# Kernel tuning notes

Measured on AMD Instinct MI355X. Metric: run time of the kernel, lower is better.

The kernel has to match this reference:

```python
import jax, jax.numpy as jnp
import numpy as np

EMBED_DIM = 1024
HEAD = 16
DK = EMBED_DIM // HEAD  # 64
B, S = 2, 2048
NEG = -1.0e9


def setup_inputs() -> dict:
    key = jax.random.key(0)
    ks = jax.random.split(key, 8)
    d = {
        'query': jax.random.normal(ks[0], (B, S, EMBED_DIM), jnp.float32),
        'key': jax.random.normal(ks[1], (B, S, EMBED_DIM), jnp.float32),
        'value': jax.random.normal(ks[2], (B, S, EMBED_DIM), jnp.float32),
        'masked': jax.random.randint(ks[3], (B, S, S), 0, 2).astype(bool),
        'Wq': jax.random.normal(ks[4], (EMBED_DIM, EMBED_DIM), jnp.float32) / np.sqrt(EMBED_DIM),
        'Wk': jax.random.normal(ks[5], (EMBED_DIM, EMBED_DIM), jnp.float32) / np.sqrt(EMBED_DIM),
        'Wv': jax.random.normal(ks[6], (EMBED_DIM, EMBED_DIM), jnp.float32) / np.sqrt(EMBED_DIM),
        'Wo': jax.random.normal(ks[7], (EMBED_DIM, EMBED_DIM), jnp.float32) / np.sqrt(EMBED_DIM),
    }
    return d


def reference(query, key, value, masked, Wq, Wk, Wv, Wo):
    # projections (bias-free Linear: x @ W), split into heads: [B, H, S, DK]
    def split_heads(x):
        b, s, _ = x.shape
        return x.reshape(b, s, HEAD, DK).transpose(0, 2, 1, 3)

    q = split_heads(query @ Wq)
    k = split_heads(key @ Wk)
    v = split_heads(value @ Wv)

    scale = 1.0 / jnp.sqrt(jnp.asarray(DK, q.dtype))
    scores = jnp.einsum('bhqd,bhkd->bhqk', q, k) * scale
    scores = jnp.where(masked[:, None, :, :], NEG, scores)
    attn = jax.nn.softmax(scores, axis=-1)
    out = jnp.einsum('bhqk,bhkd->bhqd', attn, v)  # [B, H, S, DK]
    out = out.transpose(0, 2, 1, 3).reshape(query.shape[0], -1, EMBED_DIM)
    return out @ Wo
```

## Files before the change

### kernel.cpp

```cpp
#include <hip/hip_runtime.h>
#include <hip/hip_bf16.h>

typedef float f32x4 __attribute__((ext_vector_type(4)));
typedef __bf16 bf16x8 __attribute__((ext_vector_type(8)));

__device__ __forceinline__ unsigned short f2bf(float f){
  unsigned int u = __builtin_bit_cast(unsigned int, f);
  u += 0x7fffu + ((u >> 16) & 1u);
  return (unsigned short)(u >> 16);
}
__device__ __forceinline__ float bf2f(unsigned short h){
  return __builtin_bit_cast(float, (unsigned int)h << 16);
}

__device__ __forceinline__ void glds16(const void* g, void* l){
  __builtin_amdgcn_global_load_lds((const __attribute__((address_space(1))) void*)g,
                                   (__attribute__((address_space(3))) void*)l, 16, 0, 0);
}

__device__ __forceinline__ f32x4 mfma16(bf16x8 a, bf16x8 b, f32x4 c){
  return __builtin_amdgcn_mfma_f32_16x16x32_bf16(a, b, c, 0, 0, 0);
}

#if __has_builtin(__builtin_amdgcn_exp2f)
__device__ __forceinline__ float exp2v(float x){ return __builtin_amdgcn_exp2f(x); }
#else
__device__ __forceinline__ float exp2v(float x){ return exp2f(x); }
#endif

__device__ __forceinline__ unsigned int cvtpk(float a, float b){
  unsigned int r;
  asm("v_cvt_pk_bf16_f32 %0, %1, %2" : "=v"(r) : "v"(a), "v"(b));
  return r;
}

__global__ void detect_kernel(const unsigned int* __restrict__ m, int* __restrict__ flag){
  int t = threadIdx.x;
  int bad = 0;
  for(int i = t; i < 4096; i += 256) bad |= (m[i] > 1u);
  unsigned long long b = __ballot(bad != 0);
  __shared__ int sbuf[4];
  if((t & 63) == 0) sbuf[t >> 6] = (b != 0ull);
  __syncthreads();
  if(t == 0) flag[0] = (sbuf[0] | sbuf[1] | sbuf[2] | sbuf[3]) ? 0 : 1;
}

__global__ void pack_mask_kernel(const unsigned char* __restrict__ m8,
                                 unsigned int* __restrict__ mp,
                                 const int* __restrict__ flag){
  const int wid = threadIdx.x >> 6, lane = threadIdx.x & 63;
  const int row = blockIdx.x * 4 + wid;
  const int is32 = flag[0];
  const int* m32 = (const int*)m8;
  for(int c0 = 0; c0 < 2048; c0 += 64){
    int mv = is32 ? m32[(size_t)row*2048 + c0 + lane]
                  : (int)m8[(size_t)row*2048 + c0 + lane];
    unsigned long long b = __ballot(mv != 0);
    if(lane == 0){
      mp[(size_t)row*64 + (c0 >> 5)]     = (unsigned int)b;
      mp[(size_t)row*64 + (c0 >> 5) + 1] = (unsigned int)(b >> 32);
    }
  }
}

__global__ void cvt3_kernel(const float* __restrict__ qs, const float* __restrict__ ks,
                            const float* __restrict__ vs, unsigned short* __restrict__ dst){
  const float* src = (blockIdx.y==0)?qs:(blockIdx.y==1)?ks:vs;
  unsigned short* d = dst + (size_t)blockIdx.y * 4194304;
  int i = blockIdx.x * 256 + threadIdx.x;
  const float4* s = (const float4*)src;
  float4 a = s[2*i], b = s[2*i+1];
  union { unsigned short h[8]; uint4 v; } o;
  o.h[0]=f2bf(a.x); o.h[1]=f2bf(a.y); o.h[2]=f2bf(a.z); o.h[3]=f2bf(a.w);
  o.h[4]=f2bf(b.x); o.h[5]=f2bf(b.y); o.h[6]=f2bf(b.z); o.h[7]=f2bf(b.w);
  ((uint4*)d)[i] = o.v;
}

__global__ void transW_kernel(const float* __restrict__ Wq, const float* __restrict__ Wk,
                              const float* __restrict__ Wv, const float* __restrict__ Wo,
                              unsigned short* __restrict__ WT){
  const float* W = (blockIdx.y==0)?Wq:(blockIdx.y==1)?Wk:(blockIdx.y==2)?Wv:Wo;
  const float scale = (blockIdx.y==0) ? 0.1803368801111601f : 1.0f;
  unsigned short* D = WT + (size_t)blockIdx.y * 1048576;
  int r0 = (blockIdx.x >> 4) * 64, c0 = (blockIdx.x & 15) * 64;
  __shared__ unsigned short T[64][65];
  int t = threadIdx.x;
  {
    int r = t >> 2, cb = (t & 3) * 16;
    const float4* src = (const float4*)(W + (size_t)(r0 + r) * 1024 + (c0 + cb));
    float4 v0 = src[0], v1 = src[1], v2 = src[2], v3 = src[3];
    float vals[16] = {v0.x,v0.y,v0.z,v0.w, v1.x,v1.y,v1.z,v1.w,
                      v2.x,v2.y,v2.z,v2.w, v3.x,v3.y,v3.z,v3.w};
    #pragma unroll
    for(int j=0;j<16;j++) T[cb + j][r] = f2bf(vals[j] * scale);
  }
  __syncthreads();
  {
    int c = t >> 2, rb = (t & 3) * 16;
    union { unsigned short h[16]; uint4 v[2]; } o;
    #pragma unroll
    for(int j=0;j<16;j++) o.h[j] = T[c][rb + j];
    uint4* dp = (uint4*)(D + (size_t)(c0 + c) * 1024 + (r0 + rb));
    dp[0] = o.v[0]; dp[1] = o.v[1];
  }
}

template<int OUTF32>
__global__ __launch_bounds__(256,2) void gemm_bt(
    const unsigned short* __restrict__ A0, const unsigned short* __restrict__ A1, const unsigned short* __restrict__ A2,
    const unsigned short* __restrict__ B0, const unsigned short* __restrict__ B1, const unsigned short* __restrict__ B2,
    unsigned short* __restrict__ C0, unsigned short* __restrict__ C1, unsigned short* __restrict__ C2,
    float* __restrict__ Cf)
{
  const unsigned short* A  = (blockIdx.z==0)?A0:(blockIdx.z==1)?A1:A2;
  const unsigned short* BT = (blockIdx.z==0)?B0:(blockIdx.z==1)?B1:B2;
  unsigned short* C        = (blockIdx.z==0)?C0:(blockIdx.z==1)?C1:C2;
  __shared__ unsigned short Asm[128*64];
  __shared__ unsigned short Bsm[128*64];
  const int wid = threadIdx.x >> 6, lane = threadIdx.x & 63;
  const int m0 = blockIdx.x * 128, n0 = blockIdx.y * 128;
  const int wrow = wid >> 1, wcol = wid & 1;
  const int li = lane & 15, lg = lane >> 4, li7 = lane & 7;
  f32x4 acc[4][4] = {};
  const int sr = lane >> 3;
  const int sc = lane & 7;

  for(int kt = 0; kt < 16; ++kt){
    const int kofs = kt * 64;
    #pragma unroll
    for(int i=0;i<4;i++){
      int r = wid*32 + i*8 + sr;
      int blk = sc ^ sr;
      glds16(A  + (size_t)(m0 + r)*1024 + kofs + blk*8, &Asm[(wid*32 + i*8)*64]);
      glds16(BT + (size_t)(n0 + r)*1024 + kofs + blk*8, &Bsm[(wid*32 + i*8)*64]);
    }
    __syncthreads();
    #pragma unroll
    for(int kk=0; kk<2; kk++){
      bf16x8 af[4], bfv[4];
      #pragma unroll
      for(int fm=0; fm<4; fm++){
        int row = wrow*64 + fm*16 + li;
        int blk = (kk*4 + lg) ^ li7;
        af[fm] = *(const bf16x8*)&Asm[row*64 + blk*8];
      }
      #pragma unroll
      for(int fn=0; fn<4; fn++){
        int row = wcol*64 + fn*16 + li;
        int blk = (kk*4 + lg) ^ li7;
        bfv[fn] = *(const bf16x8*)&Bsm[row*64 + blk*8];
      }
      __builtin_amdgcn_s_setprio(1);
      #pragma unroll
      for(int fm=0; fm<4; fm++)
        #pragma unroll
        for(int fn=0; fn<4; fn++)
          acc[fm][fn] = mfma16(af[fm], bfv[fn], acc[fm][fn]);
      __builtin_amdgcn_s_setprio(0);
    }
    __syncthreads();
  }
  if(OUTF32 == 0 && blockIdx.z == 2){
    #pragma unroll
    for(int fm=0; fm<4; fm++){
      #pragma unroll
      for(int fn=0; fn<4; fn++){
        int col  = n0 + wcol*64 + fn*16 + li;
        int rowb = m0 + wrow*64 + fm*16 + lg*4;
        int bq = rowb >> 11, s = rowb & 2047;
        union { unsigned short h[4]; unsigned long long u; } o;
        #pragma unroll
        for(int r=0;r<4;r++) o.h[r] = f2bf(acc[fm][fn][r]);
        *(unsigned long long*)&C[((size_t)(bq*16 + (col>>6))*64 + (col&63))*2048 + s] = o.u;
      }
    }
  } else {
    #pragma unroll
    for(int fm=0; fm<4; fm++){
      #pragma unroll
      for(int fn=0; fn<4; fn++){
        int col  = n0 + wcol*64 + fn*16 + li;
        int rowb = m0 + wrow*64 + fm*16 + lg*4;
        #pragma unroll
        for(int r=0;r<4;r++){
          if(OUTF32) Cf[(size_t)(rowb + r)*1024 + col] = acc[fm][fn][r];
          else       C [(size_t)(rowb + r)*1024 + col] = f2bf(acc[fm][fn][r]);
        }
      }
    }
  }
}

__global__ __launch_bounds__(256,4) void attn_kernel(
    const unsigned short* __restrict__ Q, const unsigned short* __restrict__ K,
    const unsigned short* __restrict__ Vt, unsigned short* __restrict__ O,
    const unsigned int* __restrict__ mp)
{
  __shared__ unsigned short Ksm[2][64*64];
  __shared__ unsigned short Vsm[2][64*64];
  const int wid = threadIdx.x >> 6, lane = threadIdx.x & 63;
  const int orig = blockIdx.x;
  const int wg = (orig & 7) * 128 + (orig >> 3);
  const int qt = wg & 31, bh = wg >> 5;
  const int b = bh >> 4, h = bh & 15;
  const int q0 = qt * 64;
  const int li = lane & 15, lg = lane >> 4;
  const int li7 = li & 7;
  const int src0 = li + 32*(lg & 1);
  const int src1 = src0 + 16;
  const int hiSel = lg >> 1;

  bf16x8 qf[2];
  {
    const unsigned short* qp = Q + (size_t)(b*2048 + q0 + wid*16 + li)*1024 + h*64 + lg*8;
    qf[0] = *(const bf16x8*)qp;
    qf[1] = *(const bf16x8*)(qp + 32);
  }

  f32x4 oacc[4] = {};
  float lrow = 0.f;

  const int srow = lane >> 3;
  const int sblk = (lane & 7) ^ srow;
  const int mrowg = b*2048 + q0 + wid*16 + li;

  #pragma unroll
  for(int i=0;i<2;i++){
    int r = wid*16 + i*8 + srow;
    glds16(K  + (size_t)(b*2048 + r)*1024 + h*64 + sblk*8, &Ksm[0][(wid*16 + i*8)*64]);
    glds16(Vt + (size_t)(bh*64 + r)*2048 + sblk*8,         &Vsm[0][(wid*16 + i*8)*64]);
  }
  uint2 mw = *(const uint2*)&mp[(size_t)mrowg*64];
  uint2 mwn;
  __syncthreads();

  int buf = 0;
  for(int t = 0; t < 32; ++t){
    const int kv0 = t * 64;
    if(t < 31){
      #pragma unroll
      for(int i=0;i<2;i++){
        int r = wid*16 + i*8 + srow;
        glds16(K  + (size_t)(b*2048 + kv0 + 64 + r)*1024 + h*64 + sblk*8, &Ksm[buf^1][(wid*16 + i*8)*64]);
        glds16(Vt + (size_t)(bh*64 + r)*2048 + kv0 + 64 + sblk*8,         &Vsm[buf^1][(wid*16 + i*8)*64]);
      }
      mwn = *(const uint2*)&mp[(size_t)mrowg*64 + (size_t)((kv0 + 64) >> 5)];
    }
    float p[4][4];
    __builtin_amdgcn_s_setprio(1);
    #pragma unroll
    for(int f=0; f<4; f++){
      f32x4 s = {0.f,0.f,0.f,0.f};
      #pragma unroll
      for(int kf=0; kf<2; kf++){
        int blk = (kf*4 + lg) ^ li7;
        bf16x8 kfr = *(const bf16x8*)&Ksm[buf][(f*16 + li)*64 + blk*8];
        s = mfma16(kfr, qf[kf], s);
      }
      #pragma unroll
      for(int j=0;j<4;j++) p[f][j] = s[j];
    }
    __builtin_amdgcn_s_setprio(0);
    unsigned int Af[4], Bf[4];
    {
      float rs = 0.f;
      #pragma unroll
      for(int f=0; f<4; f++){
        unsigned int w = (f < 2) ? mw.x : mw.y;
        float e[4];
        #pragma unroll
        for(int j=0;j<4;j++){
          unsigned int bit = (w >> ((f & 1)*16 + lg*4 + j)) & 1u;
          float v = exp2v(p[f][j]);
          e[j] = bit ? 0.f : v;
          rs += e[j];
        }
        Af[f] = cvtpk(e[0], e[1]);
        Bf[f] = cvtpk(e[2], e[3]);
      }
      lrow += rs;
    }
    #pragma unroll
    for(int ks=0; ks<2; ks++){
      unsigned int a0 = __shfl(Af[ks*2],   src0);
      unsigned int a1 = __shfl(Af[ks*2+1], src0);
      unsigned int b0 = __shfl(Bf[ks*2],   src0);
      unsigned int b1 = __shfl(Bf[ks*2+1], src0);
      unsigned int c0 = __shfl(Af[ks*2],   src1);
      unsigned int c1 = __shfl(Af[ks*2+1], src1);
      unsigned int d0 = __shfl(Bf[ks*2],   src1);
      unsigned int d1 = __shfl(Bf[ks*2+1], src1);
      union { unsigned int w[4]; bf16x8 v; } pa;
      pa.w[0] = hiSel ? a1 : a0;
      pa.w[1] = hiSel ? b1 : b0;
      pa.w[2] = hiSel ? c1 : c0;
      pa.w[3] = hiSel ? d1 : d0;
      __builtin_amdgcn_s_setprio(1);
      #pragma unroll
      for(int d=0; d<4; d++){
        int blk = (ks*4 + lg) ^ li7;
        bf16x8 vf = *(const bf16x8*)&Vsm[buf][(d*16 + li)*64 + blk*8];
        oacc[d] = mfma16(pa.v, vf, oacc[d]);
      }
      __builtin_amdgcn_s_setprio(0);
    }
    __syncthreads();
    mw = mwn;
    buf ^= 1;
  }
  float rs = lrow;
  rs += __shfl_xor(rs, 16);
  rs += __shfl_xor(rs, 32);
  float inv = 1.0f / rs;
  float io0 = __shfl(inv, lg*4 + 0);
  float io1 = __shfl(inv, lg*4 + 1);
  float io2 = __shfl(inv, lg*4 + 2);
  float io3 = __shfl(inv, lg*4 + 3);
  #pragma unroll
  for(int d=0; d<4; d++){
    size_t rb = (size_t)(b*2048 + q0 + wid*16 + lg*4);
    O[(rb+0)*1024 + h*64 + 16*d + li] = f2bf(oacc[d][0] * io0);
    O[(rb+1)*1024 + h*64 + 16*d + li] = f2bf(oacc[d][1] * io1);
    O[(rb+2)*1024 + h*64 + 16*d + li] = f2bf(oacc[d][2] * io2);
    O[(rb+3)*1024 + h*64 + 16*d + li] = f2bf(oacc[d][3] * io3);
  }
}

extern "C" void kernel_launch(void* const* d_in, const int* in_sizes, int n_in,
                              void* d_out, int out_size, void* d_ws, size_t ws_size,
                              hipStream_t stream)
{
  const float* q_in = (const float*)d_in[0];
  const float* k_in = (const float*)d_in[1];
  const float* v_in = (const float*)d_in[2];
  const unsigned char* mask = (const unsigned char*)d_in[3];
  const float* Wq = (const float*)d_in[4];
  const float* Wk = (const float*)d_in[5];
  const float* Wv = (const float*)d_in[6];
  const float* Wo = (const float*)d_in[7];

  char* ws = (char*)d_ws;
  const size_t MB = 1024*1024;
  int* flag          = (int*)ws;
  unsigned short* XQ = (unsigned short*)(ws + 256);
  unsigned short* XK = (unsigned short*)(ws + 256 + 8*MB);
  unsigned short* XV = (unsigned short*)(ws + 256 + 16*MB);
  unsigned short* WT = (unsigned short*)(ws + 256 + 24*MB);
  unsigned short* Qb = (unsigned short*)(ws + 256 + 32*MB);
  unsigned short* Kb = (unsigned short*)(ws + 256 + 40*MB);
  unsigned short* Vt = (unsigned short*)(ws + 256 + 48*MB);
  unsigned short* Ob = XQ;
  unsigned int*   mpk= (unsigned int*)XV;

  detect_kernel<<<1, 256, 0, stream>>>((const unsigned int*)mask, flag);
  cvt3_kernel<<<dim3(2048,3), 256, 0, stream>>>(q_in, k_in, v_in, XQ);
  transW_kernel<<<dim3(256,4), 256, 0, stream>>>(Wq, Wk, Wv, Wo, WT);
  gemm_bt<0><<<dim3(32,8,3), 256, 0, stream>>>(XQ, XK, XV,
                                               WT, WT + 1048576, WT + 2097152,
                                               Qb, Kb, Vt, nullptr);
  pack_mask_kernel<<<1024, 256, 0, stream>>>(mask, mpk, flag);
  attn_kernel<<<1024, 256, 0, stream>>>(Qb, Kb, Vt, Ob, mpk);
  gemm_bt<1><<<dim3(32,8,1), 256, 0, stream>>>(Ob, Ob, Ob,
                                               WT + 3*1048576, WT + 3*1048576, WT + 3*1048576,
                                               nullptr, nullptr, nullptr, (float*)d_out);
}
```

Measured before the change: 153.0 us.

## Process two query row tiles per wave and use fp16 PV MFMA without shuffles

Each attention workgroup now covers 128 query rows, with each wave handling two 16-row tiles, so every K/V tile staged in LDS is reused twice and the grid halves. Softmax probabilities are packed as fp16 and fed to the 16x16x16 f16 MFMA in the layout they already have. This removes the cross-lane shuffle permutation that the bf16 path needed. V is now written as fp16 by the projection GEMM to match. The cost is more registers (launch bounds lowered to 2), fewer blocks in flight, and fp16 range/precision for V and P.

```diff
diff --git a/kernel.cpp b/kernel.cpp
--- a/kernel.cpp
+++ b/kernel.cpp
@@ -3,6 +3,8 @@
 
 typedef float f32x4 __attribute__((ext_vector_type(4)));
 typedef __bf16 bf16x8 __attribute__((ext_vector_type(8)));
+typedef _Float16 f16x2 __attribute__((ext_vector_type(2)));
+typedef _Float16 f16x4 __attribute__((ext_vector_type(4)));
 
 __device__ __forceinline__ unsigned short f2bf(float f){
   unsigned int u = __builtin_bit_cast(unsigned int, f);
@@ -13,6 +15,10 @@
   return __builtin_bit_cast(float, (unsigned int)h << 16);
 }
 
+__device__ __forceinline__ f16x2 pkrtz(float a, float b){
+  return __builtin_bit_cast(f16x2, __builtin_amdgcn_cvt_pkrtz(a, b));
+}
+
 __device__ __forceinline__ void glds16(const void* g, void* l){
   __builtin_amdgcn_global_load_lds((const __attribute__((address_space(1))) void*)g,
                                    (__attribute__((address_space(3))) void*)l, 16, 0, 0);
@@ -20,6 +26,9 @@
 
 __device__ __forceinline__ f32x4 mfma16(bf16x8 a, bf16x8 b, f32x4 c){
   return __builtin_amdgcn_mfma_f32_16x16x32_bf16(a, b, c, 0, 0, 0);
+}
+__device__ __forceinline__ f32x4 mfma16h(f16x4 a, f16x4 b, f32x4 c){
+  return __builtin_amdgcn_mfma_f32_16x16x16f16(a, b, c, 0, 0, 0);
 }
 
 #if __has_builtin(__builtin_amdgcn_exp2f)
@@ -27,12 +36,6 @@
 #else
 __device__ __forceinline__ float exp2v(float x){ return exp2f(x); }
 #endif
-
-__device__ __forceinline__ unsigned int cvtpk(float a, float b){
-  unsigned int r;
-  asm("v_cvt_pk_bf16_f32 %0, %1, %2" : "=v"(r) : "v"(a), "v"(b));
-  return r;
-}
 
 __global__ void detect_kernel(const unsigned int* __restrict__ m, int* __restrict__ flag){
   int t = threadIdx.x;
@@ -168,9 +171,9 @@
         int col  = n0 + wcol*64 + fn*16 + li;
         int rowb = m0 + wrow*64 + fm*16 + lg*4;
         int bq = rowb >> 11, s = rowb & 2047;
-        union { unsigned short h[4]; unsigned long long u; } o;
-        #pragma unroll
-        for(int r=0;r<4;r++) o.h[r] = f2bf(acc[fm][fn][r]);
+        union { f16x2 h2[2]; unsigned long long u; } o;
+        o.h2[0] = pkrtz(acc[fm][fn][0], acc[fm][fn][1]);
+        o.h2[1] = pkrtz(acc[fm][fn][2], acc[fm][fn][3]);
         *(unsigned long long*)&C[((size_t)(bq*16 + (col>>6))*64 + (col&63))*2048 + s] = o.u;
       }
     }
@@ -191,7 +194,7 @@
   }
 }
 
-__global__ __launch_bounds__(256,4) void attn_kernel(
+__global__ __launch_bounds__(256,2) void attn_kernel(
     const unsigned short* __restrict__ Q, const unsigned short* __restrict__ K,
     const unsigned short* __restrict__ Vt, unsigned short* __restrict__ O,
     const unsigned int* __restrict__ mp)
@@ -200,29 +203,29 @@
   __shared__ unsigned short Vsm[2][64*64];
   const int wid = threadIdx.x >> 6, lane = threadIdx.x & 63;
   const int orig = blockIdx.x;
-  const int wg = (orig & 7) * 128 + (orig >> 3);
-  const int qt = wg & 31, bh = wg >> 5;
+  const int wg = (orig & 7) * 64 + (orig >> 3);
+  const int qt = wg & 15, bh = wg >> 4;
   const int b = bh >> 4, h = bh & 15;
-  const int q0 = qt * 64;
+  const int q0 = qt * 128;
   const int li = lane & 15, lg = lane >> 4;
   const int li7 = li & 7;
-  const int src0 = li + 32*(lg & 1);
-  const int src1 = src0 + 16;
-  const int hiSel = lg >> 1;
-
-  bf16x8 qf[2];
+
+  const int rowA = b*2048 + q0 + wid*32 + li;
+  const int rowB = rowA + 16;
+
+  bf16x8 qfA[2], qfB[2];
   {
-    const unsigned short* qp = Q + (size_t)(b*2048 + q0 + wid*16 + li)*1024 + h*64 + lg*8;
-    qf[0] = *(const bf16x8*)qp;
-    qf[1] = *(const bf16x8*)(qp + 32);
-  }
-
-  f32x4 oacc[4] = {};
-  float lrow = 0.f;
+    const unsigned short* qa = Q + (size_t)rowA*1024 + h*64 + lg*8;
+    const unsigned short* qb = Q + (size_t)rowB*1024 + h*64 + lg*8;
+    qfA[0] = *(const bf16x8*)qa; qfA[1] = *(const bf16x8*)(qa + 32);
+    qfB[0] = *(const bf16x8*)qb; qfB[1] = *(const bf16x8*)(qb + 32);
+  }
+
+  f32x4 oaccA[4] = {}, oaccB[4] = {};
+  float lrowA = 0.f, lrowB = 0.f;
 
   const int srow = lane >> 3;
   const int sblk = (lane & 7) ^ srow;
-  const int mrowg = b*2048 + q0 + wid*16 + li;
 
   #pragma unroll
   for(int i=0;i<2;i++){
@@ -230,8 +233,9 @@
     glds16(K  + (size_t)(b*2048 + r)*1024 + h*64 + sblk*8, &Ksm[0][(wid*16 + i*8)*64]);
     glds16(Vt + (size_t)(bh*64 + r)*2048 + sblk*8,         &Vsm[0][(wid*16 + i*8)*64]);
   }
-  uint2 mw = *(const uint2*)&mp[(size_t)mrowg*64];
-  uint2 mwn;
+  uint2 mwA = *(const uint2*)&mp[(size_t)rowA*64];
+  uint2 mwB = *(const uint2*)&mp[(size_t)rowB*64];
+  uint2 mwAn, mwBn;
   __syncthreads();
 
   int buf = 0;
@@ -244,85 +248,76 @@
         glds16(K  + (size_t)(b*2048 + kv0 + 64 + r)*1024 + h*64 + sblk*8, &Ksm[buf^1][(wid*16 + i*8)*64]);
         glds16(Vt + (size_t)(bh*64 + r)*2048 + kv0 + 64 + sblk*8,         &Vsm[buf^1][(wid*16 + i*8)*64]);
       }
-      mwn = *(const uint2*)&mp[(size_t)mrowg*64 + (size_t)((kv0 + 64) >> 5)];
-    }
-    float p[4][4];
+      mwAn = *(const uint2*)&mp[(size_t)rowA*64 + (size_t)((kv0 + 64) >> 5)];
+      mwBn = *(const uint2*)&mp[(size_t)rowB*64 + (size_t)((kv0 + 64) >> 5)];
+    }
+    f32x4 pA[4], pB[4];
     __builtin_amdgcn_s_setprio(1);
     #pragma unroll
     for(int f=0; f<4; f++){
-      f32x4 s = {0.f,0.f,0.f,0.f};
+      f32x4 sa = {0.f,0.f,0.f,0.f}, sb = {0.f,0.f,0.f,0.f};
       #pragma unroll
       for(int kf=0; kf<2; kf++){
         int blk = (kf*4 + lg) ^ li7;
         bf16x8 kfr = *(const bf16x8*)&Ksm[buf][(f*16 + li)*64 + blk*8];
-        s = mfma16(kfr, qf[kf], s);
-      }
-      #pragma unroll
-      for(int j=0;j<4;j++) p[f][j] = s[j];
+        sa = mfma16(kfr, qfA[kf], sa);
+        sb = mfma16(kfr, qfB[kf], sb);
+      }
+      pA[f] = sa; pB[f] = sb;
     }
     __builtin_amdgcn_s_setprio(0);
-    unsigned int Af[4], Bf[4];
-    {
-      float rs = 0.f;
-      #pragma unroll
-      for(int f=0; f<4; f++){
-        unsigned int w = (f < 2) ? mw.x : mw.y;
-        float e[4];
-        #pragma unroll
-        for(int j=0;j<4;j++){
-          unsigned int bit = (w >> ((f & 1)*16 + lg*4 + j)) & 1u;
-          float v = exp2v(p[f][j]);
-          e[j] = bit ? 0.f : v;
-          rs += e[j];
-        }
-        Af[f] = cvtpk(e[0], e[1]);
-        Bf[f] = cvtpk(e[2], e[3]);
-      }
-      lrow += rs;
-    }
-    #pragma unroll
-    for(int ks=0; ks<2; ks++){
-      unsigned int a0 = __shfl(Af[ks*2],   src0);
-      unsigned int a1 = __shfl(Af[ks*2+1], src0);
-      unsigned int b0 = __shfl(Bf[ks*2],   src0);
-      unsigned int b1 = __shfl(Bf[ks*2+1], src0);
-      unsigned int c0 = __shfl(Af[ks*2],   src1);
-      unsigned int c1 = __shfl(Af[ks*2+1], src1);
-      unsigned int d0 = __shfl(Bf[ks*2],   src1);
-      unsigned int d1 = __shfl(Bf[ks*2+1], src1);
-      union { unsigned int w[4]; bf16x8 v; } pa;
-      pa.w[0] = hiSel ? a1 : a0;
-      pa.w[1] = hiSel ? b1 : b0;
-      pa.w[2] = hiSel ? c1 : c0;
-      pa.w[3] = hiSel ? d1 : d0;
+    #pragma unroll
+    for(int f=0; f<4; f++){
+      unsigned int wA = (f < 2) ? mwA.x : mwA.y;
+      unsigned int wB = (f < 2) ? mwB.x : mwB.y;
+      float eA[4], eB[4];
+      #pragma unroll
+      for(int j=0;j<4;j++){
+        unsigned int bitA = (wA >> ((f & 1)*16 + lg*4 + j)) & 1u;
+        unsigned int bitB = (wB >> ((f & 1)*16 + lg*4 + j)) & 1u;
+        float vA = exp2v(pA[f][j]);
+        float vB = exp2v(pB[f][j]);
+        eA[j] = bitA ? 0.f : vA;
+        eB[j] = bitB ? 0.f : vB;
+      }
+      lrowA += (eA[0] + eA[1]) + (eA[2] + eA[3]);
+      lrowB += (eB[0] + eB[1]) + (eB[2] + eB[3]);
+      union { f16x2 h2[2]; f16x4 v; } ua, ub;
+      ua.h2[0] = pkrtz(eA[0], eA[1]);
+      ua.h2[1] = pkrtz(eA[2], eA[3]);
+      ub.h2[0] = pkrtz(eB[0], eB[1]);
+      ub.h2[1] = pkrtz(eB[2], eB[3]);
+      const int blk = (f*2 + (lg >> 1)) ^ li7;
+      const int sub = (lg & 1)*4;
       __builtin_amdgcn_s_setprio(1);
       #pragma unroll
-      for(int d=0; d<4; d++){
-        int blk = (ks*4 + lg) ^ li7;
-        bf16x8 vf = *(const bf16x8*)&Vsm[buf][(d*16 + li)*64 + blk*8];
-        oacc[d] = mfma16(pa.v, vf, oacc[d]);
+      for(int dt=0; dt<4; dt++){
+        f16x4 vf = *(const f16x4*)&Vsm[buf][(dt*16 + li)*64 + blk*8 + sub];
+        oaccA[dt] = mfma16h(ua.v, vf, oaccA[dt]);
+        oaccB[dt] = mfma16h(ub.v, vf, oaccB[dt]);
       }
       __builtin_amdgcn_s_setprio(0);
     }
     __syncthreads();
-    mw = mwn;
+    mwA = mwAn; mwB = mwBn;
     buf ^= 1;
   }
-  float rs = lrow;
-  rs += __shfl_xor(rs, 16);
-  rs += __shfl_xor(rs, 32);
-  float inv = 1.0f / rs;
-  float io0 = __shfl(inv, lg*4 + 0);
-  float io1 = __shfl(inv, lg*4 + 1);
-  float io2 = __shfl(inv, lg*4 + 2);
-  float io3 = __shfl(inv, lg*4 + 3);
+  float rsA = lrowA, rsB = lrowB;
+  rsA += __shfl_xor(rsA, 16); rsA += __shfl_xor(rsA, 32);
+  rsB += __shfl_xor(rsB, 16); rsB += __shfl_xor(rsB, 32);
+  float invA = 1.0f / rsA;
+  float invB = 1.0f / rsB;
   #pragma unroll
-  for(int d=0; d<4; d++){
-    size_t rb = (size_t)(b*2048 + q0 + wid*16 + lg*4);
-    O[(rb+0)*1024 + h*64 + 16*d + li] = f2bf(oacc[d][0] * io0);
-    O[(rb+1)*1024 + h*64 + 16*d + li] = f2bf(oacc[d][1] * io1);
-    O[(rb+2)*1024 + h*64 + 16*d + li] = f2bf(oacc[d][2] * io2);
-    O[(rb+3)*1024 + h*64 + 16*d + li] = f2bf(oacc[d][3] * io3);
+  for(int r=0;r<4;r++){
+    float ioA = __shfl(invA, lg*4 + r);
+    float ioB = __shfl(invB, lg*4 + r);
+    size_t rbA = (size_t)(b*2048 + q0 + wid*32 + lg*4 + r);
+    size_t rbB = rbA + 16;
+    #pragma unroll
+    for(int dt=0; dt<4; dt++){
+      O[rbA*1024 + h*64 + 16*dt + li] = f2bf(oaccA[dt][r] * ioA);
+      O[rbB*1024 + h*64 + 16*dt + li] = f2bf(oaccB[dt][r] * ioB);
+    }
   }
 }
 
@@ -359,7 +354,7 @@
                                                WT, WT + 1048576, WT + 2097152,
                                                Qb, Kb, Vt, nullptr);
   pack_mask_kernel<<<1024, 256, 0, stream>>>(mask, mpk, flag);
-  attn_kernel<<<1024, 256, 0, stream>>>(Qb, Kb, Vt, Ob, mpk);
+  attn_kernel<<<512, 256, 0, stream>>>(Qb, Kb, Vt, Ob, mpk);
   gemm_bt<1><<<dim3(32,8,1), 256, 0, stream>>>(Ob, Ob, Ob,
                                                WT + 3*1048576, WT + 3*1048576, WT + 3*1048576,
                                                nullptr, nullptr, nullptr, (float*)d_out);
```

After: 142.3 us. 1.08x faster.
